# Kernel tuning notes

Hardware: AMD Instinct MI355X
Metric: run time of the kernel (lower is better)

The kernel has to match this reference:

```python
import jax, jax.numpy as jnp
import numpy as np

N_NODES = 50000
N_EDGES = 1600000
IN_CH = 128
HID_CH = 32
HEADS1 = 4
OUT_CH = 64
NEG_SLOPE = 0.2


def setup_inputs() -> dict:
    key = jax.random.key(0)
    ks = jax.random.split(key, 12)
    x = jax.random.normal(ks[0], (N_NODES, IN_CH), dtype=jnp.float32)
    edge_index = jax.random.randint(ks[1], (2, N_EDGES), 0, N_NODES, dtype=jnp.int64)

    def glorot(k, shape):
        fan = shape[0] + shape[-1]
        lim = jnp.sqrt(6.0 / fan).astype(jnp.float32)
        return jax.random.uniform(k, shape, jnp.float32, -lim, lim)

    # conv1: GATConv(IN_CH, HID_CH, heads=4), concat -> HID_CH*4
    W1 = glorot(ks[2], (IN_CH, HEADS1 * HID_CH))
    a_src1 = glorot(ks[3], (HEADS1, HID_CH))
    a_dst1 = glorot(ks[4], (HEADS1, HID_CH))
    b1 = jnp.zeros((HEADS1 * HID_CH,), jnp.float32)
    # conv2: GATConv(HID_CH*4, OUT_CH, heads=1)
    W2 = glorot(ks[5], (HEADS1 * HID_CH, OUT_CH))
    a_src2 = glorot(ks[6], (1, OUT_CH))
    a_dst2 = glorot(ks[7], (1, OUT_CH))
    b2 = jnp.zeros((OUT_CH,), jnp.float32)
    return {"x": x, "edge_index": edge_index, "W1": W1, "a_src1": a_src1,
            "a_dst1": a_dst1, "b1": b1, "W2": W2, "a_src2": a_src2,
            "a_dst2": a_dst2, "b2": b2}


def gat_conv(x, src, dst, W, a_src, a_dst, b, heads, ch, concat, num_nodes):
    # linear transform per head: [N, heads, ch]
    h = (x @ W).reshape(num_nodes, heads, ch)
    # per-node attention logits: [N, heads]
    al_src = jnp.sum(h * a_src[None], axis=-1)
    al_dst = jnp.sum(h * a_dst[None], axis=-1)
    # edge-wise score e_ij = leaky_relu(al_src[j] + al_dst[i]): [E, heads]
    e = jax.nn.leaky_relu(al_src[src] + al_dst[dst], NEG_SLOPE)
    # segment softmax over incoming edges of each dst node (numerically stable)
    m = jax.ops.segment_max(e, dst, num_segments=num_nodes)
    e = jnp.exp(e - m[dst])
    s = jax.ops.segment_sum(e, dst, num_segments=num_nodes)
    alpha = e / (s[dst] + 1e-16)
    # gather source features, weight, scatter-add to dst
    msg = h[src] * alpha[:, :, None]                      # [E, heads, ch]
    out = jax.ops.segment_sum(msg, dst, num_segments=num_nodes)  # [N, heads, ch]
    out = out.reshape(num_nodes, heads * ch) if concat else out.mean(axis=1)
    return out + b


def reference(x, edge_index, W1, a_src1, a_dst1, b1, W2, a_src2, a_dst2, b2):
    n = x.shape[0]
    # add self-loops (PyG GATConv default add_self_loops=True)
    loops = jnp.arange(n, dtype=edge_index.dtype)
    src = jnp.concatenate([edge_index[0], loops])
    dst = jnp.concatenate([edge_index[1], loops])
    h = gat_conv(x, src, dst, W1, a_src1, a_dst1, b1, HEADS1, HID_CH, True, n)
    h = jax.nn.elu(h)
    out = gat_conv(h, src, dst, W2, a_src2, a_dst2, b2, 1, OUT_CH, True, n)
    return out
```

## Files before the change

kernel.cpp:

```cpp
#include <hip/hip_runtime.h>

#define NN 50000
#define NE 1600000
#define ET (NE + NN)
#define NEG 0.2f
#define NBUCK 196
#define CAP 10240
#define NBLK_A ((ET + 4095) / 4096)

typedef unsigned int uint;

__device__ __forceinline__ float bflo(uint u){ return __uint_as_float(u << 16); }
__device__ __forceinline__ float bfhi(uint u){ return __uint_as_float(u & 0xffff0000u); }
__device__ __forceinline__ uint f2bf2(float lo, float hi){
    uint a = __float_as_uint(lo); a += 0x7fffu + ((a >> 16) & 1u);
    uint b = __float_as_uint(hi); b += 0x7fffu + ((b >> 16) & 1u);
    return (a >> 16) | (b & 0xffff0000u);
}
__device__ __forceinline__ int clampn(int v){ return v < 0 ? 0 : (v >= NN ? NN - 1 : v); }

__global__ void detect_i64_kernel(const int* __restrict__ ei, int* __restrict__ flag){
    __shared__ int sd[256];
    int t = threadIdx.x;
    sd[t] = ei[2 * (t * 6250) + 1];
    __syncthreads();
    for (int o = 128; o > 0; o >>= 1){
        if (t < o) sd[t] |= sd[t + o];
        __syncthreads();
    }
    if (t == 0) *flag = (sd[0] == 0) ? 1 : 0;
}

__device__ __forceinline__ int load_src(const int* ei, int i64, int t){
    return clampn(i64 ? ei[2 * t] : ei[t]);
}
__device__ __forceinline__ int load_dst(const int* ei, int i64, int t){
    return clampn(i64 ? ei[2 * NE + 2 * t] : ei[NE + t]);
}

__global__ __launch_bounds__(256) void bucketA_kernel(const int* __restrict__ ei, const int* __restrict__ flag,
                                                      int* __restrict__ gcur, uint* __restrict__ bdata){
    __shared__ int hist[NBUCK];
    __shared__ int base[NBUCK];
    int t = threadIdx.x;
    for (int j = t; j < NBUCK; j += 256) hist[j] = 0;
    __syncthreads();
    int e0 = blockIdx.x * 4096;
    int i64 = *flag;
    uint vals[16]; int bks[16];
    #pragma unroll
    for (int j = 0; j < 16; ++j){
        int e = e0 + t + j * 256;
        if (e < ET){
            int s, d;
            if (e < NE){ s = load_src(ei, i64, e); d = load_dst(ei, i64, e); }
            else       { s = e - NE; d = s; }
            int b = d >> 8;
            bks[j] = b;
            vals[j] = ((uint)(d & 255) << 17) | (uint)s;
            atomicAdd(&hist[b], 1);
        } else bks[j] = -1;
    }
    __syncthreads();
    for (int j = t; j < NBUCK; j += 256){
        int c = hist[j];
        base[j] = c ? atomicAdd(&gcur[j], c) : 0;
        hist[j] = 0;
    }
    __syncthreads();
    #pragma unroll
    for (int j = 0; j < 16; ++j){
        int b = bks[j];
        if (b >= 0){
            int lp = base[b] + atomicAdd(&hist[b], 1);
            if (lp < CAP) bdata[(size_t)b * CAP + lp] = vals[j];
        }
    }
}

__global__ __launch_bounds__(256) void bucketB_kernel(const uint* __restrict__ bdata, const int* __restrict__ gcur,
                                                      int* __restrict__ offsets, int* __restrict__ ends,
                                                      int* __restrict__ csr){
    __shared__ int hist[256];
    __shared__ int excl[256];
    __shared__ int sgb;
    int b = blockIdx.x, t = threadIdx.x;
    int cv = (t < NBUCK) ? gcur[t] : 0; if (cv > CAP) cv = CAP;
    excl[t] = cv;
    __syncthreads();
    for (int o = 1; o < 256; o <<= 1){
        int x = (t >= o) ? excl[t - o] : 0;
        __syncthreads();
        excl[t] += x;
        __syncthreads();
    }
    if (t == b) sgb = excl[t] - cv;
    __syncthreads();
    int gb = sgb;
    int n = gcur[b]; if (n > CAP) n = CAP;
    hist[t] = 0;
    __syncthreads();
    const uint* bd = bdata + (size_t)b * CAP;
    for (int i = t; i < n; i += 256)
        atomicAdd(&hist[bd[i] >> 17], 1);
    __syncthreads();
    int v = hist[t];
    excl[t] = v;
    __syncthreads();
    for (int o = 1; o < 256; o <<= 1){
        int x = (t >= o) ? excl[t - o] : 0;
        __syncthreads();
        excl[t] += x;
        __syncthreads();
    }
    int ex = excl[t] - v;
    int node = b * 256 + t;
    if (node < NN){ offsets[node] = gb + ex; ends[node] = gb + ex + v; }
    __syncthreads();
    hist[t] = ex;
    __syncthreads();
    for (int i = t; i < n; i += 256){
        uint val = bd[i];
        int lp = atomicAdd(&hist[val >> 17], 1);
        csr[gb + lp] = (int)(val & 0x1FFFFu);
    }
}

__global__ __launch_bounds__(256) void gemm1_kernel(const float* __restrict__ x, const float* __restrict__ W1,
                                                    const float* __restrict__ as1, const float* __restrict__ ad1,
                                                    uint* __restrict__ h1b, float* __restrict__ als,
                                                    float* __restrict__ ald){
    __shared__ float Ws[128 * 128];
    __shared__ float xs[32 * 128];
    int t = threadIdx.x;
    const float4* W4 = (const float4*)W1;
    float4* Ws4 = (float4*)Ws;
    #pragma unroll
    for (int j = 0; j < 16; ++j){ int idx = t + j * 256; Ws4[idx] = W4[idx]; }
    int row0 = blockIdx.x * 32;
    const float4* x4 = (const float4*)x;
    float4* xs4 = (float4*)xs;
    #pragma unroll
    for (int j = 0; j < 4; ++j){
        int idx = t + j * 256;
        int gi = row0 * 32 + idx;
        if (gi < NN * 32) xs4[idx] = x4[gi];
    }
    __syncthreads();
    int rg = t >> 5, cg = t & 31;
    float acc[4][4];
    #pragma unroll
    for (int i = 0; i < 4; ++i)
        #pragma unroll
        for (int c = 0; c < 4; ++c) acc[i][c] = 0.f;
    const float4* WsR = (const float4*)Ws;
    for (int k4 = 0; k4 < 32; ++k4){
        int k = k4 * 4;
        float4 xv[4];
        #pragma unroll
        for (int i = 0; i < 4; ++i) xv[i] = xs4[(rg * 4 + i) * 32 + k4];
        float4 w0 = WsR[(k + 0) * 32 + cg];
        float4 w1 = WsR[(k + 1) * 32 + cg];
        float4 w2 = WsR[(k + 2) * 32 + cg];
        float4 w3 = WsR[(k + 3) * 32 + cg];
        #pragma unroll
        for (int i = 0; i < 4; ++i){
            acc[i][0] = fmaf(xv[i].x, w0.x, acc[i][0]);
            acc[i][1] = fmaf(xv[i].x, w0.y, acc[i][1]);
            acc[i][2] = fmaf(xv[i].x, w0.z, acc[i][2]);
            acc[i][3] = fmaf(xv[i].x, w0.w, acc[i][3]);
            acc[i][0] = fmaf(xv[i].y, w1.x, acc[i][0]);
            acc[i][1] = fmaf(xv[i].y, w1.y, acc[i][1]);
            acc[i][2] = fmaf(xv[i].y, w1.z, acc[i][2]);
            acc[i][3] = fmaf(xv[i].y, w1.w, acc[i][3]);
            acc[i][0] = fmaf(xv[i].z, w2.x, acc[i][0]);
            acc[i][1] = fmaf(xv[i].z, w2.y, acc[i][1]);
            acc[i][2] = fmaf(xv[i].z, w2.z, acc[i][2]);
            acc[i][3] = fmaf(xv[i].z, w2.w, acc[i][3]);
            acc[i][0] = fmaf(xv[i].w, w3.x, acc[i][0]);
            acc[i][1] = fmaf(xv[i].w, w3.y, acc[i][1]);
            acc[i][2] = fmaf(xv[i].w, w3.z, acc[i][2]);
            acc[i][3] = fmaf(xv[i].w, w3.w, acc[i][3]);
        }
    }
    int h = cg >> 3, c0 = (cg & 7) * 4;
    const float* ash = as1 + h * 32 + c0;
    const float* adh = ad1 + h * 32 + c0;
    float as0 = ash[0], as1v = ash[1], as2v = ash[2], as3v = ash[3];
    float ad0 = adh[0], ad1v = adh[1], ad2v = adh[2], ad3v = adh[3];
    #pragma unroll
    for (int i = 0; i < 4; ++i){
        int n = row0 + rg * 4 + i;
        if (n < NN){
            ((uint2*)h1b)[n * 32 + cg] = make_uint2(f2bf2(acc[i][0], acc[i][1]),
                                                    f2bf2(acc[i][2], acc[i][3]));
            float ps = acc[i][0] * as0 + acc[i][1] * as1v + acc[i][2] * as2v + acc[i][3] * as3v;
            float pd = acc[i][0] * ad0 + acc[i][1] * ad1v + acc[i][2] * ad2v + acc[i][3] * ad3v;
            ps += __shfl_xor(ps, 1); pd += __shfl_xor(pd, 1);
            ps += __shfl_xor(ps, 2); pd += __shfl_xor(pd, 2);
            ps += __shfl_xor(ps, 4); pd += __shfl_xor(pd, 4);
            if ((cg & 7) == 0){ als[n * 4 + h] = ps; ald[n * 4 + h] = pd; }
        }
    }
}

__global__ __launch_bounds__(256) void edge1_kernel(const int* __restrict__ offs, const int* __restrict__ ends,
                                                    const int* __restrict__ csr, const uint* __restrict__ h1b,
                                                    const float* __restrict__ als, const float* __restrict__ ald,
                                                    const float* __restrict__ b1, uint* __restrict__ helub){
    __shared__ int   ss[4][64];
    __shared__ float sw[4][64][4];
    int t = threadIdx.x, wave = t >> 6, lane = t & 63;
    int node = blockIdx.x * 4 + wave;
    int begin = offs[node], end = ends[node];
    int deg = end - begin;
    int eg = lane >> 4, cl = lane & 15, hh = cl >> 2;
    float4 ad = ((const float4*)ald)[node];
    const float4* als4 = (const float4*)als;
    const uint4* h1b4 = (const uint4*)h1b;

    float ws0 = 0, ws1 = 0, ws2 = 0, ws3 = 0;
    float acc[8];
    #pragma unroll
    for (int i = 0; i < 8; ++i) acc[i] = 0.f;
    bool fast = (deg <= 64);

    if (fast){
        float w0 = 0, w1 = 0, w2 = 0, w3 = 0;
        int s0 = 0;
        if (lane < deg){
            s0 = csr[begin + lane];
            float4 a = als4[s0];
            float e0 = a.x + ad.x; e0 = e0 > 0.f ? e0 : NEG * e0; w0 = __expf(e0);
            float e1 = a.y + ad.y; e1 = e1 > 0.f ? e1 : NEG * e1; w1 = __expf(e1);
            float e2 = a.z + ad.z; e2 = e2 > 0.f ? e2 : NEG * e2; w2 = __expf(e2);
            float e3 = a.w + ad.w; e3 = e3 > 0.f ? e3 : NEG * e3; w3 = __expf(e3);
            ws0 = w0; ws1 = w1; ws2 = w2; ws3 = w3;
        }
        ss[wave][lane] = s0;
        sw[wave][lane][0] = w0; sw[wave][lane][1] = w1;
        sw[wave][lane][2] = w2; sw[wave][lane][3] = w3;
        __threadfence_block();
        int dlim = (deg + 3) & ~3;
        int j = 0;
        for (; j + 16 <= dlim; j += 16){
            int sj[4]; float wj[4]; uint4 v[4];
            #pragma unroll
            for (int q = 0; q < 4; ++q){
                sj[q] = ss[wave][j + 4 * q + eg];
                wj[q] = sw[wave][j + 4 * q + eg][hh];
            }
            #pragma unroll
            for (int q = 0; q < 4; ++q) v[q] = h1b4[(size_t)sj[q] * 16 + cl];
            #pragma unroll
            for (int q = 0; q < 4; ++q){
                acc[0] = fmaf(wj[q], bflo(v[q].x), acc[0]);
                acc[1] = fmaf(wj[q], bfhi(v[q].x), acc[1]);
                acc[2] = fmaf(wj[q], bflo(v[q].y), acc[2]);
                acc[3] = fmaf(wj[q], bfhi(v[q].y), acc[3]);
                acc[4] = fmaf(wj[q], bflo(v[q].z), acc[4]);
                acc[5] = fmaf(wj[q], bfhi(v[q].z), acc[5]);
                acc[6] = fmaf(wj[q], bflo(v[q].w), acc[6]);
                acc[7] = fmaf(wj[q], bfhi(v[q].w), acc[7]);
            }
        }
        for (; j < dlim; j += 4){
            int sj = ss[wave][j + eg]; float wj = sw[wave][j + eg][hh];
            uint4 v = h1b4[(size_t)sj * 16 + cl];
            acc[0] = fmaf(wj, bflo(v.x), acc[0]);
            acc[1] = fmaf(wj, bfhi(v.x), acc[1]);
            acc[2] = fmaf(wj, bflo(v.y), acc[2]);
            acc[3] = fmaf(wj, bfhi(v.y), acc[3]);
            acc[4] = fmaf(wj, bflo(v.z), acc[4]);
            acc[5] = fmaf(wj, bfhi(v.z), acc[5]);
            acc[6] = fmaf(wj, bflo(v.w), acc[6]);
            acc[7] = fmaf(wj, bfhi(v.w), acc[7]);
        }
    } else {
        for (int base = begin; base < end; base += 64){
            int n = end - base; if (n > 64) n = 64;
            float w0 = 0, w1 = 0, w2 = 0, w3 = 0; int sv = 0;
            if (lane < n){
                sv = csr[base + lane];
                float4 a = als4[sv];
                float f0 = a.x + ad.x; f0 = f0 > 0.f ? f0 : NEG * f0; w0 = __expf(f0);
                float f1 = a.y + ad.y; f1 = f1 > 0.f ? f1 : NEG * f1; w1 = __expf(f1);
                float f2 = a.z + ad.z; f2 = f2 > 0.f ? f2 : NEG * f2; w2 = __expf(f2);
                float f3 = a.w + ad.w; f3 = f3 > 0.f ? f3 : NEG * f3; w3 = __expf(f3);
                ws0 += w0; ws1 += w1; ws2 += w2; ws3 += w3;
            }
            __threadfence_block();
            ss[wave][lane] = sv;
            sw[wave][lane][0] = w0; sw[wave][lane][1] = w1;
            sw[wave][lane][2] = w2; sw[wave][lane][3] = w3;
            __threadfence_block();
            int dlim = (n + 3) & ~3;
            for (int j = 0; j < dlim; j += 4){
                int sj = ss[wave][j + eg]; float wj = sw[wave][j + eg][hh];
                uint4 v = h1b4[(size_t)sj * 16 + cl];
                acc[0] = fmaf(wj, bflo(v.x), acc[0]);
                acc[1] = fmaf(wj, bfhi(v.x), acc[1]);
                acc[2] = fmaf(wj, bflo(v.y), acc[2]);
                acc[3] = fmaf(wj, bfhi(v.y), acc[3]);
                acc[4] = fmaf(wj, bflo(v.z), acc[4]);
                acc[5] = fmaf(wj, bfhi(v.z), acc[5]);
                acc[6] = fmaf(wj, bflo(v.w), acc[6]);
                acc[7] = fmaf(wj, bfhi(v.w), acc[7]);
            }
        }
    }
    for (int o = 32; o > 0; o >>= 1){
        ws0 += __shfl_xor(ws0, o); ws1 += __shfl_xor(ws1, o);
        ws2 += __shfl_xor(ws2, o); ws3 += __shfl_xor(ws3, o);
    }
    #pragma unroll
    for (int i = 0; i < 8; ++i){
        acc[i] += __shfl_xor(acc[i], 16);
        acc[i] += __shfl_xor(acc[i], 32);
    }
    if (eg == 0){
        float wsum = hh == 0 ? ws0 : (hh == 1 ? ws1 : (hh == 2 ? ws2 : ws3));
        float inv = 1.f / (wsum + 1e-16f);
        int c0 = cl * 8;
        float o[8];
        #pragma unroll
        for (int i = 0; i < 8; ++i){
            float v = acc[i] * inv + b1[c0 + i];
            o[i] = v > 0.f ? v : __expf(v) - 1.f;
        }
        uint4 pk = make_uint4(f2bf2(o[0], o[1]), f2bf2(o[2], o[3]),
                              f2bf2(o[4], o[5]), f2bf2(o[6], o[7]));
        ((uint4*)helub)[(size_t)node * 16 + cl] = pk;
    }
}

__global__ __launch_bounds__(256) void gemm2_kernel(const uint* __restrict__ helub, const float* __restrict__ W2,
                                                    const float* __restrict__ as2, const float* __restrict__ ad2,
                                                    uint* __restrict__ h2b, float* __restrict__ als2,
                                                    float* __restrict__ ald2){
    __shared__ float W2s[128 * 64];
    __shared__ uint  hsu[64 * 65];
    int t = threadIdx.x;
    const float4* W24 = (const float4*)W2;
    float4* W2s4 = (float4*)W2s;
    #pragma unroll
    for (int j = 0; j < 8; ++j){ int idx = t + j * 256; W2s4[idx] = W24[idx]; }
    int row0 = blockIdx.x * 64;
    const uint4* hb4 = (const uint4*)helub;
    #pragma unroll
    for (int j = 0; j < 4; ++j){
        int idx = t + j * 256;
        int gi = row0 * 16 + idx;
        if (gi < NN * 16){
            uint4 v = hb4[gi];
            int r = idx >> 4, kq = idx & 15;
            uint* dst = hsu + r * 65 + kq * 4;
            dst[0] = v.x; dst[1] = v.y; dst[2] = v.z; dst[3] = v.w;
        }
    }
    __syncthreads();
    int rg = t >> 4, cg = t & 15;
    float acc[4][4];
    #pragma unroll
    for (int i = 0; i < 4; ++i)
        #pragma unroll
        for (int c = 0; c < 4; ++c) acc[i][c] = 0.f;
    const float4* W2sR = (const float4*)W2s;
    for (int k2 = 0; k2 < 64; ++k2){
        uint hv[4];
        #pragma unroll
        for (int i = 0; i < 4; ++i) hv[i] = hsu[(rg * 4 + i) * 65 + k2];
        float4 wa = W2sR[(2 * k2) * 16 + cg];
        float4 wb = W2sR[(2 * k2 + 1) * 16 + cg];
        #pragma unroll
        for (int i = 0; i < 4; ++i){
            float xl = bflo(hv[i]), xh = bfhi(hv[i]);
            acc[i][0] = fmaf(xl, wa.x, acc[i][0]);
            acc[i][1] = fmaf(xl, wa.y, acc[i][1]);
            acc[i][2] = fmaf(xl, wa.z, acc[i][2]);
            acc[i][3] = fmaf(xl, wa.w, acc[i][3]);
            acc[i][0] = fmaf(xh, wb.x, acc[i][0]);
            acc[i][1] = fmaf(xh, wb.y, acc[i][1]);
            acc[i][2] = fmaf(xh, wb.z, acc[i][2]);
            acc[i][3] = fmaf(xh, wb.w, acc[i][3]);
        }
    }
    int c0 = cg * 4;
    float s0 = as2[c0], s1 = as2[c0 + 1], s2 = as2[c0 + 2], s3 = as2[c0 + 3];
    float d0 = ad2[c0], d1 = ad2[c0 + 1], d2 = ad2[c0 + 2], d3 = ad2[c0 + 3];
    #pragma unroll
    for (int i = 0; i < 4; ++i){
        int n = row0 + rg * 4 + i;
        if (n < NN){
            ((uint2*)h2b)[n * 16 + cg] = make_uint2(f2bf2(acc[i][0], acc[i][1]),
                                                    f2bf2(acc[i][2], acc[i][3]));
            float ps = acc[i][0] * s0 + acc[i][1] * s1 + acc[i][2] * s2 + acc[i][3] * s3;
            float pd = acc[i][0] * d0 + acc[i][1] * d1 + acc[i][2] * d2 + acc[i][3] * d3;
            ps += __shfl_xor(ps, 1); pd += __shfl_xor(pd, 1);
            ps += __shfl_xor(ps, 2); pd += __shfl_xor(pd, 2);
            ps += __shfl_xor(ps, 4); pd += __shfl_xor(pd, 4);
            ps += __shfl_xor(ps, 8); pd += __shfl_xor(pd, 8);
            if (cg == 0){ als2[n] = ps; ald2[n] = pd; }
        }
    }
}

__global__ __launch_bounds__(256) void edge2_kernel(const int* __restrict__ offs, const int* __restrict__ ends,
                                                    const int* __restrict__ csr, const uint* __restrict__ h2b,
                                                    const float* __restrict__ als, const float* __restrict__ ald,
                                                    const float* __restrict__ b2, float* __restrict__ out){
    __shared__ int   ss2[4][64];
    __shared__ float sw2[4][64];
    int t = threadIdx.x, wave = t >> 6, lane = t & 63;
    int node = blockIdx.x * 4 + wave;
    int begin = offs[node], end = ends[node];
    int deg = end - begin;
    int eg = lane >> 4, cl = lane & 15;
    float adv = ald[node];
    const uint2* h2p = (const uint2*)h2b;
    float wsl = 0.f;
    float acc[4] = {0.f, 0.f, 0.f, 0.f};
    bool fast = (deg <= 64);
    if (fast){
        float w = 0.f; int sv = 0;
        if (lane < deg){
            sv = csr[begin + lane];
            float e = als[sv] + adv; e = e > 0.f ? e : NEG * e;
            w = __expf(e); wsl = w;
        }
        ss2[wave][lane] = sv;
        sw2[wave][lane] = w;
        __threadfence_block();
        int dlim = (deg + 3) & ~3;
        int j = 0;
        for (; j + 16 <= dlim; j += 16){
            int sj[4]; float wj[4]; uint2 v[4];
            #pragma unroll
            for (int q = 0; q < 4; ++q){
                sj[q] = ss2[wave][j + 4 * q + eg];
                wj[q] = sw2[wave][j + 4 * q + eg];
            }
            #pragma unroll
            for (int q = 0; q < 4; ++q) v[q] = h2p[(size_t)sj[q] * 16 + cl];
            #pragma unroll
            for (int q = 0; q < 4; ++q){
                acc[0] = fmaf(wj[q], bflo(v[q].x), acc[0]);
                acc[1] = fmaf(wj[q], bfhi(v[q].x), acc[1]);
                acc[2] = fmaf(wj[q], bflo(v[q].y), acc[2]);
                acc[3] = fmaf(wj[q], bfhi(v[q].y), acc[3]);
            }
        }
        for (; j < dlim; j += 4){
            int sj = ss2[wave][j + eg]; float wj = sw2[wave][j + eg];
            uint2 v = h2p[(size_t)sj * 16 + cl];
            acc[0] = fmaf(wj, bflo(v.x), acc[0]);
            acc[1] = fmaf(wj, bfhi(v.x), acc[1]);
            acc[2] = fmaf(wj, bflo(v.y), acc[2]);
            acc[3] = fmaf(wj, bfhi(v.y), acc[3]);
        }
    } else {
        for (int base = begin; base < end; base += 64){
            int n = end - base; if (n > 64) n = 64;
            float w = 0.f; int sv = 0;
            if (lane < n){
                sv = csr[base + lane];
                float e = als[sv] + adv; e = e > 0.f ? e : NEG * e;
                w = __expf(e); wsl += w;
            }
            __threadfence_block();
            ss2[wave][lane] = sv;
            sw2[wave][lane] = w;
            __threadfence_block();
            int dlim = (n + 3) & ~3;
            for (int j = 0; j < dlim; j += 4){
                int sj = ss2[wave][j + eg]; float wj = sw2[wave][j + eg];
                uint2 v = h2p[(size_t)sj * 16 + cl];
                acc[0] = fmaf(wj, bflo(v.x), acc[0]);
                acc[1] = fmaf(wj, bfhi(v.x), acc[1]);
                acc[2] = fmaf(wj, bflo(v.y), acc[2]);
                acc[3] = fmaf(wj, bfhi(v.y), acc[3]);
            }
        }
    }
    for (int o = 32; o > 0; o >>= 1) wsl += __shfl_xor(wsl, o);
    #pragma unroll
    for (int i = 0; i < 4; ++i){
        acc[i] += __shfl_xor(acc[i], 16);
        acc[i] += __shfl_xor(acc[i], 32);
    }
    if (eg == 0){
        float inv = 1.f / (wsl + 1e-16f);
        int c0 = cl * 4;
        ((float4*)out)[node * 16 + cl] = make_float4(acc[0] * inv + b2[c0],
                                                     acc[1] * inv + b2[c0 + 1],
                                                     acc[2] * inv + b2[c0 + 2],
                                                     acc[3] * inv + b2[c0 + 3]);
    }
}


extern "C" void kernel_launch(void* const* d_in, const int* in_sizes, int n_in,
                              void* d_out, int out_size, void* d_ws, size_t ws_size,
                              hipStream_t stream){
    const float* x   = (const float*)d_in[0];
    const int*   ei  = (const int*)d_in[1];
    const float* W1  = (const float*)d_in[2];
    const float* as1 = (const float*)d_in[3];
    const float* ad1 = (const float*)d_in[4];
    const float* b1  = (const float*)d_in[5];
    const float* W2  = (const float*)d_in[6];
    const float* as2 = (const float*)d_in[7];
    const float* ad2 = (const float*)d_in[8];
    const float* b2  = (const float*)d_in[9];
    float* out = (float*)d_out;

    char* p = (char*)d_ws;
    auto alloc = [&](size_t bytes)->void*{
        void* r = (void*)p;
        p += (bytes + 255) & ~(size_t)255;
        return r;
    };
    int*   flag     = (int*)alloc(4);
    int*   gcur     = (int*)alloc(NBUCK * 4);
    int*   offsets  = (int*)alloc(NN * 4);
    int*   endsv    = (int*)alloc(NN * 4);
    void*  ualias   = alloc((size_t)NN * 64 * 4);
    uint*  bdata    = (uint*)ualias;
    uint*  helub    = (uint*)ualias;
    int*   csr      = (int*)alloc((size_t)ET * 4);
    uint*  h1b      = (uint*)alloc((size_t)NN * 64 * 4);
    float* als1     = (float*)alloc((size_t)NN * 4 * 4);
    float* ald1     = (float*)alloc((size_t)NN * 4 * 4);
    uint*  h2b      = (uint*)alloc((size_t)NN * 32 * 4);
    float* als2     = (float*)alloc((size_t)NN * 4);
    float* ald2     = (float*)alloc((size_t)NN * 4);
    size_t need = (size_t)(p - (char*)d_ws);

    if (ws_size < need){
        hipMemsetAsync(d_out, 0, (size_t)out_size * 4, stream);
        return;
    }

    hipMemsetAsync(gcur, 0, NBUCK * 4, stream);
    detect_i64_kernel<<<1, 256, 0, stream>>>(ei, flag);
    bucketA_kernel<<<NBLK_A, 256, 0, stream>>>(ei, flag, gcur, bdata);
    bucketB_kernel<<<NBUCK, 256, 0, stream>>>(bdata, gcur, offsets, endsv, csr);

    gemm1_kernel<<<(NN + 31) / 32, 256, 0, stream>>>(x, W1, as1, ad1, h1b, als1, ald1);
    edge1_kernel<<<NN / 4, 256, 0, stream>>>(offsets, endsv, csr, h1b, als1, ald1, b1, helub);
    gemm2_kernel<<<(NN + 63) / 64, 256, 0, stream>>>(helub, W2, as2, ad2, h2b, als2, ald2);
    edge2_kernel<<<NN / 4, 256, 0, stream>>>(offsets, endsv, csr, h2b, als2, ald2, b2, out);
}
```

Measured before the change: 277.6 us.

## Co-schedule bucketing with gemm1, vectorize edge loads, widen edge2 gathers

```diff
diff --git a/kernel.cpp b/kernel.cpp
--- a/kernel.cpp
+++ b/kernel.cpp
@@ -7,6 +7,8 @@
 #define NBUCK 196
 #define CAP 10240
 #define NBLK_A ((ET + 4095) / 4096)
+#define G1_BLOCKS ((NN + 31) / 32)
+#define G1_SPLIT 782
 
 typedef unsigned int uint;
 
@@ -19,9 +21,17 @@
 }
 __device__ __forceinline__ int clampn(int v){ return v < 0 ? 0 : (v >= NN ? NN - 1 : v); }
 
-__global__ void detect_i64_kernel(const int* __restrict__ ei, int* __restrict__ flag){
+__device__ __forceinline__ int load_src(const int* ei, int i64, int t){
+    return clampn(i64 ? ei[2 * t] : ei[t]);
+}
+__device__ __forceinline__ int load_dst(const int* ei, int i64, int t){
+    return clampn(i64 ? ei[2 * NE + 2 * t] : ei[NE + t]);
+}
+
+__global__ void setup_kernel(const int* __restrict__ ei, int* __restrict__ flag, int* __restrict__ gcur){
     __shared__ int sd[256];
     int t = threadIdx.x;
+    if (t < NBUCK) gcur[t] = 0;
     sd[t] = ei[2 * (t * 6250) + 1];
     __syncthreads();
     for (int o = 128; o > 0; o >>= 1){
@@ -31,34 +41,55 @@
     if (t == 0) *flag = (sd[0] == 0) ? 1 : 0;
 }
 
-__device__ __forceinline__ int load_src(const int* ei, int i64, int t){
-    return clampn(i64 ? ei[2 * t] : ei[t]);
-}
-__device__ __forceinline__ int load_dst(const int* ei, int i64, int t){
-    return clampn(i64 ? ei[2 * NE + 2 * t] : ei[NE + t]);
-}
-
-__global__ __launch_bounds__(256) void bucketA_kernel(const int* __restrict__ ei, const int* __restrict__ flag,
-                                                      int* __restrict__ gcur, uint* __restrict__ bdata){
-    __shared__ int hist[NBUCK];
-    __shared__ int base[NBUCK];
+__device__ __forceinline__ void bucketA_body(char* smem, int b, const int* __restrict__ ei,
+                                             const int* __restrict__ flag, int* __restrict__ gcur,
+                                             uint* __restrict__ bdata){
+    int* hist = (int*)smem;
+    int* base = hist + NBUCK;
     int t = threadIdx.x;
     for (int j = t; j < NBUCK; j += 256) hist[j] = 0;
     __syncthreads();
-    int e0 = blockIdx.x * 4096;
+    int e0 = b * 4096;
     int i64 = *flag;
+    int sarr[16], darr[16];
+    if (e0 + 4096 <= NE){
+        int eb = e0 + t * 16;
+        if (i64){
+            const int4* s4 = (const int4*)ei + (eb >> 1);
+            const int4* d4 = (const int4*)(ei + 2 * NE) + (eb >> 1);
+            #pragma unroll
+            for (int q = 0; q < 8; ++q){
+                int4 v = s4[q]; sarr[2*q] = v.x; sarr[2*q+1] = v.z;
+                int4 w = d4[q]; darr[2*q] = w.x; darr[2*q+1] = w.z;
+            }
+        } else {
+            const int4* s4 = (const int4*)ei + (eb >> 2);
+            const int4* d4 = (const int4*)(ei + NE) + (eb >> 2);
+            #pragma unroll
+            for (int q = 0; q < 4; ++q){
+                int4 v = s4[q]; sarr[4*q]=v.x; sarr[4*q+1]=v.y; sarr[4*q+2]=v.z; sarr[4*q+3]=v.w;
+                int4 w = d4[q]; darr[4*q]=w.x; darr[4*q+1]=w.y; darr[4*q+2]=w.z; darr[4*q+3]=w.w;
+            }
+        }
+        #pragma unroll
+        for (int j = 0; j < 16; ++j){ sarr[j] = clampn(sarr[j]); darr[j] = clampn(darr[j]); }
+    } else {
+        #pragma unroll
+        for (int j = 0; j < 16; ++j){
+            int e = e0 + t * 16 + j;
+            if (e < NE){ sarr[j] = load_src(ei, i64, e); darr[j] = load_dst(ei, i64, e); }
+            else if (e < ET){ sarr[j] = e - NE; darr[j] = e - NE; }
+            else { sarr[j] = -1; darr[j] = -1; }
+        }
+    }
     uint vals[16]; int bks[16];
     #pragma unroll
     for (int j = 0; j < 16; ++j){
-        int e = e0 + t + j * 256;
-        if (e < ET){
-            int s, d;
-            if (e < NE){ s = load_src(ei, i64, e); d = load_dst(ei, i64, e); }
-            else       { s = e - NE; d = s; }
-            int b = d >> 8;
-            bks[j] = b;
-            vals[j] = ((uint)(d & 255) << 17) | (uint)s;
-            atomicAdd(&hist[b], 1);
+        if (darr[j] >= 0){
+            int bk = darr[j] >> 8;
+            bks[j] = bk;
+            vals[j] = ((uint)(darr[j] & 255) << 17) | (uint)sarr[j];
+            atomicAdd(&hist[bk], 1);
         } else bks[j] = -1;
     }
     __syncthreads();
@@ -70,21 +101,21 @@
     __syncthreads();
     #pragma unroll
     for (int j = 0; j < 16; ++j){
-        int b = bks[j];
-        if (b >= 0){
-            int lp = base[b] + atomicAdd(&hist[b], 1);
-            if (lp < CAP) bdata[(size_t)b * CAP + lp] = vals[j];
-        }
-    }
-}
-
-__global__ __launch_bounds__(256) void bucketB_kernel(const uint* __restrict__ bdata, const int* __restrict__ gcur,
-                                                      int* __restrict__ offsets, int* __restrict__ ends,
-                                                      int* __restrict__ csr){
-    __shared__ int hist[256];
-    __shared__ int excl[256];
-    __shared__ int sgb;
-    int b = blockIdx.x, t = threadIdx.x;
+        int bk = bks[j];
+        if (bk >= 0){
+            int lp = base[bk] + atomicAdd(&hist[bk], 1);
+            if (lp < CAP) bdata[(size_t)bk * CAP + lp] = vals[j];
+        }
+    }
+}
+
+__device__ __forceinline__ void bucketB_body(char* smem, int b, const uint* __restrict__ bdata,
+                                             const int* __restrict__ gcur, int* __restrict__ offsets,
+                                             int* __restrict__ ends, int* __restrict__ csr){
+    int* hist = (int*)smem;
+    int* excl = hist + 256;
+    int* sgb  = excl + 256;
+    int t = threadIdx.x;
     int cv = (t < NBUCK) ? gcur[t] : 0; if (cv > CAP) cv = CAP;
     excl[t] = cv;
     __syncthreads();
@@ -94,9 +125,9 @@
         excl[t] += x;
         __syncthreads();
     }
-    if (t == b) sgb = excl[t] - cv;
-    __syncthreads();
-    int gb = sgb;
+    if (t == b) *sgb = excl[t] - cv;
+    __syncthreads();
+    int gb = *sgb;
     int n = gcur[b]; if (n > CAP) n = CAP;
     hist[t] = 0;
     __syncthreads();
@@ -126,18 +157,18 @@
     }
 }
 
-__global__ __launch_bounds__(256) void gemm1_kernel(const float* __restrict__ x, const float* __restrict__ W1,
-                                                    const float* __restrict__ as1, const float* __restrict__ ad1,
-                                                    uint* __restrict__ h1b, float* __restrict__ als,
-                                                    float* __restrict__ ald){
-    __shared__ float Ws[128 * 128];
-    __shared__ float xs[32 * 128];
+__device__ __forceinline__ void gemm1_body(char* smem, int gb, const float* __restrict__ x,
+                                           const float* __restrict__ W1, const float* __restrict__ as1,
+                                           const float* __restrict__ ad1, uint* __restrict__ h1b,
+                                           float* __restrict__ als, float* __restrict__ ald){
+    float* Ws = (float*)smem;
+    float* xs = Ws + 128 * 128;
     int t = threadIdx.x;
     const float4* W4 = (const float4*)W1;
     float4* Ws4 = (float4*)Ws;
     #pragma unroll
     for (int j = 0; j < 16; ++j){ int idx = t + j * 256; Ws4[idx] = W4[idx]; }
-    int row0 = blockIdx.x * 32;
+    int row0 = gb * 32;
     const float4* x4 = (const float4*)x;
     float4* xs4 = (float4*)xs;
     #pragma unroll
@@ -204,6 +235,29 @@
     }
 }
 
+__global__ __launch_bounds__(256) void k1_kernel(const int* __restrict__ ei, const int* __restrict__ flag,
+                                                 int* __restrict__ gcur, uint* __restrict__ bdata,
+                                                 const float* __restrict__ x, const float* __restrict__ W1,
+                                                 const float* __restrict__ as1, const float* __restrict__ ad1,
+                                                 uint* __restrict__ h1b, float* __restrict__ als,
+                                                 float* __restrict__ ald){
+    __shared__ __align__(16) char smem[128 * 128 * 4 + 32 * 128 * 4];
+    if ((int)blockIdx.x < NBLK_A) bucketA_body(smem, blockIdx.x, ei, flag, gcur, bdata);
+    else gemm1_body(smem, blockIdx.x - NBLK_A, x, W1, as1, ad1, h1b, als, ald);
+}
+
+__global__ __launch_bounds__(256) void k2_kernel(const uint* __restrict__ bdata, const int* __restrict__ gcur,
+                                                 int* __restrict__ offsets, int* __restrict__ ends,
+                                                 int* __restrict__ csr,
+                                                 const float* __restrict__ x, const float* __restrict__ W1,
+                                                 const float* __restrict__ as1, const float* __restrict__ ad1,
+                                                 uint* __restrict__ h1b, float* __restrict__ als,
+                                                 float* __restrict__ ald){
+    __shared__ __align__(16) char smem[128 * 128 * 4 + 32 * 128 * 4];
+    if ((int)blockIdx.x < NBUCK) bucketB_body(smem, blockIdx.x, bdata, gcur, offsets, ends, csr);
+    else gemm1_body(smem, blockIdx.x - NBUCK + G1_SPLIT, x, W1, as1, ad1, h1b, als, ald);
+}
+
 __global__ __launch_bounds__(256) void edge1_kernel(const int* __restrict__ offs, const int* __restrict__ ends,
                                                     const int* __restrict__ csr, const uint* __restrict__ h1b,
                                                     const float* __restrict__ als, const float* __restrict__ ald,
@@ -415,11 +469,11 @@
     int node = blockIdx.x * 4 + wave;
     int begin = offs[node], end = ends[node];
     int deg = end - begin;
-    int eg = lane >> 4, cl = lane & 15;
+    int eg = lane >> 3, cl = lane & 7;
     float adv = ald[node];
-    const uint2* h2p = (const uint2*)h2b;
+    const uint4* h2p4 = (const uint4*)h2b;
     float wsl = 0.f;
-    float acc[4] = {0.f, 0.f, 0.f, 0.f};
+    float acc[8] = {0.f, 0.f, 0.f, 0.f, 0.f, 0.f, 0.f, 0.f};
     bool fast = (deg <= 64);
     if (fast){
         float w = 0.f; int sv = 0;
@@ -431,32 +485,29 @@
         ss2[wave][lane] = sv;
         sw2[wave][lane] = w;
         __threadfence_block();
-        int dlim = (deg + 3) & ~3;
+        int dlim = (deg + 7) & ~7;
         int j = 0;
         for (; j + 16 <= dlim; j += 16){
-            int sj[4]; float wj[4]; uint2 v[4];
-            #pragma unroll
-            for (int q = 0; q < 4; ++q){
-                sj[q] = ss2[wave][j + 4 * q + eg];
-                wj[q] = sw2[wave][j + 4 * q + eg];
-            }
-            #pragma unroll
-            for (int q = 0; q < 4; ++q) v[q] = h2p[(size_t)sj[q] * 16 + cl];
-            #pragma unroll
-            for (int q = 0; q < 4; ++q){
-                acc[0] = fmaf(wj[q], bflo(v[q].x), acc[0]);
-                acc[1] = fmaf(wj[q], bfhi(v[q].x), acc[1]);
-                acc[2] = fmaf(wj[q], bflo(v[q].y), acc[2]);
-                acc[3] = fmaf(wj[q], bfhi(v[q].y), acc[3]);
-            }
-        }
-        for (; j < dlim; j += 4){
+            int sj0 = ss2[wave][j + eg],     sj1 = ss2[wave][j + 8 + eg];
+            float wj0 = sw2[wave][j + eg],   wj1 = sw2[wave][j + 8 + eg];
+            uint4 v0 = h2p4[(size_t)sj0 * 8 + cl];
+            uint4 v1 = h2p4[(size_t)sj1 * 8 + cl];
+            acc[0] = fmaf(wj0, bflo(v0.x), acc[0]); acc[1] = fmaf(wj0, bfhi(v0.x), acc[1]);
+            acc[2] = fmaf(wj0, bflo(v0.y), acc[2]); acc[3] = fmaf(wj0, bfhi(v0.y), acc[3]);
+            acc[4] = fmaf(wj0, bflo(v0.z), acc[4]); acc[5] = fmaf(wj0, bfhi(v0.z), acc[5]);
+            acc[6] = fmaf(wj0, bflo(v0.w), acc[6]); acc[7] = fmaf(wj0, bfhi(v0.w), acc[7]);
+            acc[0] = fmaf(wj1, bflo(v1.x), acc[0]); acc[1] = fmaf(wj1, bfhi(v1.x), acc[1]);
+            acc[2] = fmaf(wj1, bflo(v1.y), acc[2]); acc[3] = fmaf(wj1, bfhi(v1.y), acc[3]);
+            acc[4] = fmaf(wj1, bflo(v1.z), acc[4]); acc[5] = fmaf(wj1, bfhi(v1.z), acc[5]);
+            acc[6] = fmaf(wj1, bflo(v1.w), acc[6]); acc[7] = fmaf(wj1, bfhi(v1.w), acc[7]);
+        }
+        for (; j < dlim; j += 8){
             int sj = ss2[wave][j + eg]; float wj = sw2[wave][j + eg];
-            uint2 v = h2p[(size_t)sj * 16 + cl];
-            acc[0] = fmaf(wj, bflo(v.x), acc[0]);
-            acc[1] = fmaf(wj, bfhi(v.x), acc[1]);
-            acc[2] = fmaf(wj, bflo(v.y), acc[2]);
-            acc[3] = fmaf(wj, bfhi(v.y), acc[3]);
+            uint4 v = h2p4[(size_t)sj * 8 + cl];
+            acc[0] = fmaf(wj, bflo(v.x), acc[0]); acc[1] = fmaf(wj, bfhi(v.x), acc[1]);
+            acc[2] = fmaf(wj, bflo(v.y), acc[2]); acc[3] = fmaf(wj, bfhi(v.y), acc[3]);
+            acc[4] = fmaf(wj, bflo(v.z), acc[4]); acc[5] = fmaf(wj, bfhi(v.z), acc[5]);
+            acc[6] = fmaf(wj, bflo(v.w), acc[6]); acc[7] = fmaf(wj, bfhi(v.w), acc[7]);
         }
     } else {
         for (int base = begin; base < end; base += 64){
@@ -471,30 +522,35 @@
             ss2[wave][lane] = sv;
             sw2[wave][lane] = w;
             __threadfence_block();
-            int dlim = (n + 3) & ~3;
-            for (int j = 0; j < dlim; j += 4){
+            int dlim = (n + 7) & ~7;
+            for (int j = 0; j < dlim; j += 8){
                 int sj = ss2[wave][j + eg]; float wj = sw2[wave][j + eg];
-                uint2 v = h2p[(size_t)sj * 16 + cl];
-                acc[0] = fmaf(wj, bflo(v.x), acc[0]);
-                acc[1] = fmaf(wj, bfhi(v.x), acc[1]);
-                acc[2] = fmaf(wj, bflo(v.y), acc[2]);
-                acc[3] = fmaf(wj, bfhi(v.y), acc[3]);
+                uint4 v = h2p4[(size_t)sj * 8 + cl];
+                acc[0] = fmaf(wj, bflo(v.x), acc[0]); acc[1] = fmaf(wj, bfhi(v.x), acc[1]);
+                acc[2] = fmaf(wj, bflo(v.y), acc[2]); acc[3] = fmaf(wj, bfhi(v.y), acc[3]);
+                acc[4] = fmaf(wj, bflo(v.z), acc[4]); acc[5] = fmaf(wj, bfhi(v.z), acc[5]);
+                acc[6] = fmaf(wj, bflo(v.w), acc[6]); acc[7] = fmaf(wj, bfhi(v.w), acc[7]);
             }
         }
     }
     for (int o = 32; o > 0; o >>= 1) wsl += __shfl_xor(wsl, o);
     #pragma unroll
-    for (int i = 0; i < 4; ++i){
+    for (int i = 0; i < 8; ++i){
+        acc[i] += __shfl_xor(acc[i], 8);
         acc[i] += __shfl_xor(acc[i], 16);
         acc[i] += __shfl_xor(acc[i], 32);
     }
     if (eg == 0){
         float inv = 1.f / (wsl + 1e-16f);
-        int c0 = cl * 4;
-        ((float4*)out)[node * 16 + cl] = make_float4(acc[0] * inv + b2[c0],
-                                                     acc[1] * inv + b2[c0 + 1],
-                                                     acc[2] * inv + b2[c0 + 2],
-                                                     acc[3] * inv + b2[c0 + 3]);
+        int c0 = cl * 8;
+        ((float4*)out)[node * 16 + cl * 2]     = make_float4(acc[0] * inv + b2[c0],
+                                                             acc[1] * inv + b2[c0 + 1],
+                                                             acc[2] * inv + b2[c0 + 2],
+                                                             acc[3] * inv + b2[c0 + 3]);
+        ((float4*)out)[node * 16 + cl * 2 + 1] = make_float4(acc[4] * inv + b2[c0 + 4],
+                                                             acc[5] * inv + b2[c0 + 5],
+                                                             acc[6] * inv + b2[c0 + 6],
+                                                             acc[7] * inv + b2[c0 + 7]);
     }
 }
 
@@ -541,12 +597,11 @@
         return;
     }
 
-    hipMemsetAsync(gcur, 0, NBUCK * 4, stream);
-    detect_i64_kernel<<<1, 256, 0, stream>>>(ei, flag);
-    bucketA_kernel<<<NBLK_A, 256, 0, stream>>>(ei, flag, gcur, bdata);
-    bucketB_kernel<<<NBUCK, 256, 0, stream>>>(bdata, gcur, offsets, endsv, csr);
-
-    gemm1_kernel<<<(NN + 31) / 32, 256, 0, stream>>>(x, W1, as1, ad1, h1b, als1, ald1);
+    setup_kernel<<<1, 256, 0, stream>>>(ei, flag, gcur);
+    k1_kernel<<<NBLK_A + G1_SPLIT, 256, 0, stream>>>(ei, flag, gcur, bdata,
+                                                     x, W1, as1, ad1, h1b, als1, ald1);
+    k2_kernel<<<NBUCK + (G1_BLOCKS - G1_SPLIT), 256, 0, stream>>>(bdata, gcur, offsets, endsv, csr,
+                                                                  x, W1, as1, ad1, h1b, als1, ald1);
     edge1_kernel<<<NN / 4, 256, 0, stream>>>(offsets, endsv, csr, h1b, als1, ald1, b1, helub);
     gemm2_kernel<<<(NN + 63) / 64, 256, 0, stream>>>(helub, W2, as2, ad2, h2b, als2, ald2);
     edge2_kernel<<<NN / 4, 256, 0, stream>>>(offsets, endsv, csr, h2b, als2, ald2, b2, out);
```

Result: faster. 254.9 us (-8.2%).
